# Kernel optimization log

Hardware: AMD Instinct MI355X
Metric: run time of the kernel (lower is better)

Reference implementation:

```python
import jax, jax.numpy as jnp
import numpy as np


def _quantize(m):
    # per-row symmetric int8 quantization: absmax over last dim, round to nearest-even
    max_val = jnp.max(jnp.abs(m), axis=-1)          # [...]
    q = jnp.round(m * (127.0 / max_val)[..., None])  # values in [-127, 127], kept in fp32
    return q, max_val


def setup_inputs() -> dict:
    key = jax.random.key(0)
    k1, k2, k3 = jax.random.split(key, 3)
    B, S, D_IN, D_OUT = 4, 8192, 1024, 1024
    x = jax.random.normal(k1, (B, S, D_IN), dtype=jnp.float32)
    weight = jax.random.normal(k2, (D_OUT, D_IN), dtype=jnp.float32) * 0.02
    bias = jax.random.normal(k3, (D_OUT,), dtype=jnp.float32)
    return {"x": x, "weight": weight, "bias": bias}


def reference(x, weight, bias):
    # weight quantization happens once in __init__; replicated here for self-containment
    w_q, w_max = _quantize(weight)    # [N,K], [N]
    x_q, x_max = _quantize(x)         # [B,S,K], [B,S]
    # int8 GEMM emulated in fp32, exactly as the original module does
    res_q = jnp.einsum('bsk,nk->bsn', x_q, w_q)            # [B,S,N] fp32
    mx = x_max[..., None] * w_max                          # outer-product dequant scale [B,S,N]
    res = (res_q / (127.0 * 127.0)).astype(jnp.float16) * mx  # fp16 * fp32 -> fp32
    return res + bias
```

## Files before the change

### kernel.cpp

```cpp
#include <hip/hip_runtime.h>
#include <hip/hip_fp16.h>


typedef int i32x4 __attribute__((ext_vector_type(4)));

#define BM 128
#define BN 128
#define BKB 128

__global__ __launch_bounds__(256) void quant_rows_kernel(
    const float* __restrict__ in, signed char* __restrict__ q,
    float* __restrict__ rowmax, int K, int R) {
  const int row = blockIdx.x;
  const int t = threadIdx.x;
  const size_t base = (size_t)row * K;
  float4 v = reinterpret_cast<const float4*>(in + base)[t];
  float a = fmaxf(fmaxf(fabsf(v.x), fabsf(v.y)), fmaxf(fabsf(v.z), fabsf(v.w)));
#pragma unroll
  for (int off = 32; off > 0; off >>= 1) a = fmaxf(a, __shfl_xor(a, off, 64));
  __shared__ float smax[4];
  if ((t & 63) == 0) smax[t >> 6] = a;
  __syncthreads();
  float m = fmaxf(fmaxf(smax[0], smax[1]), fmaxf(smax[2], smax[3]));
  float s = 127.0f / m;
  char4 qq;
  qq.x = (signed char)(int)rintf(v.x * s);
  qq.y = (signed char)(int)rintf(v.y * s);
  qq.z = (signed char)(int)rintf(v.z * s);
  qq.w = (signed char)(int)rintf(v.w * s);
  const int kb = t >> 5;
  signed char* dst =
      q + (size_t)kb * R * BKB + (size_t)row * BKB + (t & 31) * 4;
  *reinterpret_cast<char4*>(dst) = qq;
  if (t == 0) rowmax[row] = m;
}

__device__ __forceinline__ void gload_lds16(const void* g, void* l) {
  __builtin_amdgcn_global_load_lds(
      (const __attribute__((address_space(1))) unsigned char*)g,
      (__attribute__((address_space(3))) unsigned char*)l, 16, 0, 0);
}

__global__ __launch_bounds__(256) void w8x8_gemm_kernel(
    const signed char* __restrict__ Aq, const signed char* __restrict__ Bq,
    const float* __restrict__ Amax, const float* __restrict__ Bmax,
    const float* __restrict__ bias, float* __restrict__ out,
    int M, int N, int K, int cpx) {
  __shared__ __align__(16) signed char ldsA[2][BM * BKB];
  __shared__ __align__(16) signed char ldsB[2][BN * BKB];
  const int t = threadIdx.x;
  const int lane = t & 63;
  const int wave = t >> 6;
  const int wrow = wave >> 1, wcol = wave & 1;

  const int nbn = N / BN;
  const int bid = blockIdx.x;
  const int tile = (bid & 7) * cpx + (bid >> 3);
  const int bm = tile / nbn, bn = tile % nbn;

  const size_t kbStrideA = (size_t)M * BKB;
  const size_t kbStrideB = (size_t)N * BKB;
  const signed char* Abase = Aq + (size_t)bm * BM * BKB;
  const signed char* Bbase = Bq + (size_t)bn * BN * BKB;

  const int soff = (t * 16) ^ (((t >> 3) & 7) << 4);

  const int fr = lane & 15, fq = lane >> 4;
  int aoff[4][2], boff[4][2];
#pragma unroll
  for (int m = 0; m < 4; ++m) {
    int ra = wrow * 64 + m * 16 + fr;
    int rb = wcol * 64 + m * 16 + fr;
#pragma unroll
    for (int ks = 0; ks < 2; ++ks) {
      aoff[m][ks] = ra * BKB + (((ks << 2) | fq) ^ (ra & 7)) * 16;
      boff[m][ks] = rb * BKB + (((ks << 2) | fq) ^ (rb & 7)) * 16;
    }
  }

  i32x4 acc[4][4];
#pragma unroll
  for (int m = 0; m < 4; ++m)
#pragma unroll
    for (int n = 0; n < 4; ++n) acc[m][n] = (i32x4){0, 0, 0, 0};

#define STAGE(bf, kt)                                                        \
  do {                                                                       \
    const signed char* ga = Abase + (size_t)(kt)*kbStrideA;                  \
    const signed char* gb = Bbase + (size_t)(kt)*kbStrideB;                  \
    gload_lds16(ga + soff, &ldsA[bf][t * 16]);                               \
    gload_lds16(ga + 4096 + soff, &ldsA[bf][4096 + t * 16]);                 \
    gload_lds16(ga + 8192 + soff, &ldsA[bf][8192 + t * 16]);                 \
    gload_lds16(ga + 12288 + soff, &ldsA[bf][12288 + t * 16]);               \
    gload_lds16(gb + soff, &ldsB[bf][t * 16]);                               \
    gload_lds16(gb + 4096 + soff, &ldsB[bf][4096 + t * 16]);                 \
    gload_lds16(gb + 8192 + soff, &ldsB[bf][8192 + t * 16]);                 \
    gload_lds16(gb + 12288 + soff, &ldsB[bf][12288 + t * 16]);               \
  } while (0)

  const int NT = K / BKB;
  STAGE(0, 0);
  asm volatile("s_waitcnt vmcnt(0)" ::: "memory");
  __builtin_amdgcn_s_barrier();

  for (int kt = 0; kt < NT; ++kt) {
    const signed char* lA = ldsA[kt & 1];
    const signed char* lB = ldsB[kt & 1];
    const bool pf = (kt + 1 < NT);
    if (pf) STAGE((kt + 1) & 1, kt + 1);

#pragma unroll
    for (int ks = 0; ks < 2; ++ks) {
      i32x4 a[4], b[4];
#pragma unroll
      for (int m = 0; m < 4; ++m) {
        a[m] = *reinterpret_cast<const i32x4*>(lA + aoff[m][ks]);
        b[m] = *reinterpret_cast<const i32x4*>(lB + boff[m][ks]);
      }
      __builtin_amdgcn_s_setprio(1);
#pragma unroll
      for (int m = 0; m < 4; ++m)
#pragma unroll
        for (int n = 0; n < 4; ++n)
          acc[m][n] = __builtin_amdgcn_mfma_i32_16x16x64_i8(a[m], b[n],
                                                            acc[m][n], 0, 0, 0);
      __builtin_amdgcn_s_setprio(0);
    }

    if (pf) {
      asm volatile("s_waitcnt vmcnt(0)" ::: "memory");
      __builtin_amdgcn_s_barrier();
    }
  }
#undef STAGE

  const int row0 = bm * BM + wrow * 64;
  const int col0 = bn * BN + wcol * 64;
  const float C = 1.0f / 16129.0f;
  float wmx[4], bs[4];
#pragma unroll
  for (int n = 0; n < 4; ++n) {
    int col = col0 + n * 16 + fr;
    wmx[n] = Bmax[col];
    bs[n] = bias[col];
  }
#pragma unroll
  for (int m = 0; m < 4; ++m) {
#pragma unroll
    for (int r = 0; r < 4; ++r) {
      int row = row0 + m * 16 + fq * 4 + r;
      float xm = Amax[row];
      float* orow = out + (size_t)row * N;
#pragma unroll
      for (int n = 0; n < 4; ++n) {
        float v = (float)acc[m][n][r] * C;
        float h = __half2float(__float2half_rn(v));
        orow[col0 + n * 16 + fr] = h * (xm * wmx[n]) + bs[n];
      }
    }
  }
}

extern "C" void kernel_launch(void* const* d_in, const int* in_sizes, int n_in,
                              void* d_out, int out_size, void* d_ws, size_t ws_size,
                              hipStream_t stream) {
  const float* x = (const float*)d_in[0];
  const float* w = (const float*)d_in[1];
  const float* bias = (const float*)d_in[2];
  float* out = (float*)d_out;

  const int N = in_sizes[2];
  const int K = in_sizes[1] / N;
  const int M = in_sizes[0] / K;

  signed char* xq = (signed char*)d_ws;
  signed char* wq = xq + (size_t)M * K;
  float* xmax = (float*)(wq + (size_t)N * K);
  float* wmax = xmax + M;

  quant_rows_kernel<<<M, 256, 0, stream>>>(x, xq, xmax, K, M);
  quant_rows_kernel<<<N, 256, 0, stream>>>(w, wq, wmax, K, N);

  const int nwg = (M / BM) * (N / BN);
  const int cpx = nwg / 8;
  w8x8_gemm_kernel<<<nwg, 256, 0, stream>>>(xq, wq, xmax, wmax, bias, out,
                                            M, N, K, cpx);
}
```

Before: 95.12 us.

## Use 256x256 tiles, 8 waves, triple-buffered K=64 pipeline with interleaved prefetch

Tiles grow to 256x256 with 512 threads. Each wave computes a 64x128 sub-tile, and the K step shrinks to 64 bytes. Shared memory now holds three buffers, with loads issued two K-steps ahead and split into A and B halves that are interleaved between MFMA groups under barriers. The quantized layout is rebuilt for 64-byte K blocks. This aims at better operand reuse and keeping the matrix units fed, at the cost of more barriers, higher register pressure and lower occupancy.

```diff
diff --git a/kernel.cpp b/kernel.cpp
--- a/kernel.cpp
+++ b/kernel.cpp
@@ -4,9 +4,9 @@
 
 typedef int i32x4 __attribute__((ext_vector_type(4)));
 
-#define BM 128
-#define BN 128
-#define BKB 128
+#define BM 256
+#define BN 256
+#define KB 64
 
 __global__ __launch_bounds__(256) void quant_rows_kernel(
     const float* __restrict__ in, signed char* __restrict__ q,
@@ -28,9 +28,8 @@
   qq.y = (signed char)(int)rintf(v.y * s);
   qq.z = (signed char)(int)rintf(v.z * s);
   qq.w = (signed char)(int)rintf(v.w * s);
-  const int kb = t >> 5;
-  signed char* dst =
-      q + (size_t)kb * R * BKB + (size_t)row * BKB + (t & 31) * 4;
+  const int kb = t >> 4;
+  signed char* dst = q + (size_t)kb * R * KB + (size_t)row * KB + (t & 15) * 4;
   *reinterpret_cast<char4*>(dst) = qq;
   if (t == 0) rowmax[row] = m;
 }
@@ -41,105 +40,147 @@
       (__attribute__((address_space(3))) unsigned char*)l, 16, 0, 0);
 }
 
-__global__ __launch_bounds__(256) void w8x8_gemm_kernel(
+__global__ __launch_bounds__(512) void w8x8_gemm_kernel(
     const signed char* __restrict__ Aq, const signed char* __restrict__ Bq,
     const float* __restrict__ Amax, const float* __restrict__ Bmax,
     const float* __restrict__ bias, float* __restrict__ out,
     int M, int N, int K, int cpx) {
-  __shared__ __align__(16) signed char ldsA[2][BM * BKB];
-  __shared__ __align__(16) signed char ldsB[2][BN * BKB];
+  __shared__ __align__(16) signed char ldsA[3][BM * KB];
+  __shared__ __align__(16) signed char ldsB[3][BN * KB];
   const int t = threadIdx.x;
   const int lane = t & 63;
   const int wave = t >> 6;
-  const int wrow = wave >> 1, wcol = wave & 1;
+  const int wm = wave >> 1;
+  const int wn = wave & 1;
 
   const int nbn = N / BN;
   const int bid = blockIdx.x;
   const int tile = (bid & 7) * cpx + (bid >> 3);
   const int bm = tile / nbn, bn = tile % nbn;
 
-  const size_t kbStrideA = (size_t)M * BKB;
-  const size_t kbStrideB = (size_t)N * BKB;
-  const signed char* Abase = Aq + (size_t)bm * BM * BKB;
-  const signed char* Bbase = Bq + (size_t)bn * BN * BKB;
-
-  const int soff = (t * 16) ^ (((t >> 3) & 7) << 4);
+  const size_t kbA = (size_t)M * KB;
+  const size_t kbB = (size_t)N * KB;
+  const signed char* Abase = Aq + (size_t)bm * BM * KB;
+  const signed char* Bbase = Bq + (size_t)bn * BN * KB;
+
+  const int ssoff = (t * 16) ^ (((t >> 3) & 3) << 4);
+  const int sdst = t * 16;
 
   const int fr = lane & 15, fq = lane >> 4;
-  int aoff[4][2], boff[4][2];
-#pragma unroll
-  for (int m = 0; m < 4; ++m) {
-    int ra = wrow * 64 + m * 16 + fr;
-    int rb = wcol * 64 + m * 16 + fr;
-#pragma unroll
-    for (int ks = 0; ks < 2; ++ks) {
-      aoff[m][ks] = ra * BKB + (((ks << 2) | fq) ^ (ra & 7)) * 16;
-      boff[m][ks] = rb * BKB + (((ks << 2) | fq) ^ (rb & 7)) * 16;
-    }
+  const int xr = (fr >> 1) & 3;
+  int aoff[4], boff[8];
+#pragma unroll
+  for (int m = 0; m < 4; ++m)
+    aoff[m] = (wm * 64 + m * 16 + fr) * KB + ((fq ^ xr) << 4);
+#pragma unroll
+  for (int n = 0; n < 8; ++n)
+    boff[n] = (wn * 128 + n * 16 + fr) * KB + ((fq ^ xr) << 4);
+
+  i32x4 acc[4][8];
+#pragma unroll
+  for (int m = 0; m < 4; ++m)
+#pragma unroll
+    for (int n = 0; n < 8; ++n) acc[m][n] = (i32x4){0, 0, 0, 0};
+
+#define STAGE_A(bf, kt)                                                    \
+  do {                                                                    \
+    const signed char* ga = Abase + (size_t)(kt) * kbA;                   \
+    gload_lds16(ga + ssoff, &ldsA[bf][sdst]);                             \
+    gload_lds16(ga + 8192 + ssoff, &ldsA[bf][8192 + sdst]);               \
+  } while (0)
+#define STAGE_B(bf, kt)                                                    \
+  do {                                                                    \
+    const signed char* gb = Bbase + (size_t)(kt) * kbB;                   \
+    gload_lds16(gb + ssoff, &ldsB[bf][sdst]);                             \
+    gload_lds16(gb + 8192 + ssoff, &ldsB[bf][8192 + sdst]);               \
+  } while (0)
+
+  const int NT = K / KB;
+  STAGE_A(0, 0);
+  STAGE_B(0, 0);
+  STAGE_A(1, 1);
+  STAGE_B(1, 1);
+  asm volatile("s_waitcnt vmcnt(4)" ::: "memory");
+  __builtin_amdgcn_s_barrier();
+
+  int cb = 0;
+  for (int kt = 0; kt < NT; ++kt) {
+    const signed char* lA = ldsA[cb];
+    const signed char* lB = ldsB[cb];
+    int sb = cb + 2;
+    if (sb >= 3) sb -= 3;
+    const bool p2 = (kt + 2 < NT), p1 = (kt + 1 < NT);
+
+    i32x4 a[4], b0, b1;
+#pragma unroll
+    for (int m = 0; m < 4; ++m)
+      a[m] = *reinterpret_cast<const i32x4*>(lA + aoff[m]);
+    b0 = *reinterpret_cast<const i32x4*>(lB + boff[0]);
+    b1 = *reinterpret_cast<const i32x4*>(lB + boff[1]);
+    if (p2) STAGE_A(sb, kt + 2);
+    __builtin_amdgcn_s_barrier();
+    __builtin_amdgcn_s_setprio(1);
+#pragma unroll
+    for (int m = 0; m < 4; ++m) {
+      acc[m][0] = __builtin_amdgcn_mfma_i32_16x16x64_i8(a[m], b0, acc[m][0], 0, 0, 0);
+      acc[m][1] = __builtin_amdgcn_mfma_i32_16x16x64_i8(a[m], b1, acc[m][1], 0, 0, 0);
+    }
+    __builtin_amdgcn_s_setprio(0);
+    __builtin_amdgcn_s_barrier();
+
+    b0 = *reinterpret_cast<const i32x4*>(lB + boff[2]);
+    b1 = *reinterpret_cast<const i32x4*>(lB + boff[3]);
+    if (p2) STAGE_B(sb, kt + 2);
+    __builtin_amdgcn_s_barrier();
+    __builtin_amdgcn_s_setprio(1);
+#pragma unroll
+    for (int m = 0; m < 4; ++m) {
+      acc[m][2] = __builtin_amdgcn_mfma_i32_16x16x64_i8(a[m], b0, acc[m][2], 0, 0, 0);
+      acc[m][3] = __builtin_amdgcn_mfma_i32_16x16x64_i8(a[m], b1, acc[m][3], 0, 0, 0);
+    }
+    __builtin_amdgcn_s_setprio(0);
+    __builtin_amdgcn_s_barrier();
+
+    b0 = *reinterpret_cast<const i32x4*>(lB + boff[4]);
+    b1 = *reinterpret_cast<const i32x4*>(lB + boff[5]);
+    __builtin_amdgcn_s_barrier();
+    __builtin_amdgcn_s_setprio(1);
+#pragma unroll
+    for (int m = 0; m < 4; ++m) {
+      acc[m][4] = __builtin_amdgcn_mfma_i32_16x16x64_i8(a[m], b0, acc[m][4], 0, 0, 0);
+      acc[m][5] = __builtin_amdgcn_mfma_i32_16x16x64_i8(a[m], b1, acc[m][5], 0, 0, 0);
+    }
+    __builtin_amdgcn_s_setprio(0);
+    __builtin_amdgcn_s_barrier();
+
+    b0 = *reinterpret_cast<const i32x4*>(lB + boff[6]);
+    b1 = *reinterpret_cast<const i32x4*>(lB + boff[7]);
+    __builtin_amdgcn_s_barrier();
+    __builtin_amdgcn_s_setprio(1);
+#pragma unroll
+    for (int m = 0; m < 4; ++m) {
+      acc[m][6] = __builtin_amdgcn_mfma_i32_16x16x64_i8(a[m], b0, acc[m][6], 0, 0, 0);
+      acc[m][7] = __builtin_amdgcn_mfma_i32_16x16x64_i8(a[m], b1, acc[m][7], 0, 0, 0);
+    }
+    __builtin_amdgcn_s_setprio(0);
+    if (p1) {
+      if (p2)
+        asm volatile("s_waitcnt vmcnt(4)" ::: "memory");
+      else
+        asm volatile("s_waitcnt vmcnt(0)" ::: "memory");
+    }
+    __builtin_amdgcn_s_barrier();
+    cb = (cb + 1 == 3) ? 0 : cb + 1;
   }
-
-  i32x4 acc[4][4];
-#pragma unroll
-  for (int m = 0; m < 4; ++m)
-#pragma unroll
-    for (int n = 0; n < 4; ++n) acc[m][n] = (i32x4){0, 0, 0, 0};
-
-#define STAGE(bf, kt)                                                        \
-  do {                                                                       \
-    const signed char* ga = Abase + (size_t)(kt)*kbStrideA;                  \
-    const signed char* gb = Bbase + (size_t)(kt)*kbStrideB;                  \
-    gload_lds16(ga + soff, &ldsA[bf][t * 16]);                               \
-    gload_lds16(ga + 4096 + soff, &ldsA[bf][4096 + t * 16]);                 \
-    gload_lds16(ga + 8192 + soff, &ldsA[bf][8192 + t * 16]);                 \
-    gload_lds16(ga + 12288 + soff, &ldsA[bf][12288 + t * 16]);               \
-    gload_lds16(gb + soff, &ldsB[bf][t * 16]);                               \
-    gload_lds16(gb + 4096 + soff, &ldsB[bf][4096 + t * 16]);                 \
-    gload_lds16(gb + 8192 + soff, &ldsB[bf][8192 + t * 16]);                 \
-    gload_lds16(gb + 12288 + soff, &ldsB[bf][12288 + t * 16]);               \
-  } while (0)
-
-  const int NT = K / BKB;
-  STAGE(0, 0);
-  asm volatile("s_waitcnt vmcnt(0)" ::: "memory");
-  __builtin_amdgcn_s_barrier();
-
-  for (int kt = 0; kt < NT; ++kt) {
-    const signed char* lA = ldsA[kt & 1];
-    const signed char* lB = ldsB[kt & 1];
-    const bool pf = (kt + 1 < NT);
-    if (pf) STAGE((kt + 1) & 1, kt + 1);
-
-#pragma unroll
-    for (int ks = 0; ks < 2; ++ks) {
-      i32x4 a[4], b[4];
-#pragma unroll
-      for (int m = 0; m < 4; ++m) {
-        a[m] = *reinterpret_cast<const i32x4*>(lA + aoff[m][ks]);
-        b[m] = *reinterpret_cast<const i32x4*>(lB + boff[m][ks]);
-      }
-      __builtin_amdgcn_s_setprio(1);
-#pragma unroll
-      for (int m = 0; m < 4; ++m)
-#pragma unroll
-        for (int n = 0; n < 4; ++n)
-          acc[m][n] = __builtin_amdgcn_mfma_i32_16x16x64_i8(a[m], b[n],
-                                                            acc[m][n], 0, 0, 0);
-      __builtin_amdgcn_s_setprio(0);
-    }
-
-    if (pf) {
-      asm volatile("s_waitcnt vmcnt(0)" ::: "memory");
-      __builtin_amdgcn_s_barrier();
-    }
-  }
-#undef STAGE
-
-  const int row0 = bm * BM + wrow * 64;
-  const int col0 = bn * BN + wcol * 64;
+#undef STAGE_A
+#undef STAGE_B
+
+  const int row0 = bm * BM + wm * 64;
+  const int col0 = bn * BN + wn * 128;
   const float C = 1.0f / 16129.0f;
-  float wmx[4], bs[4];
-#pragma unroll
-  for (int n = 0; n < 4; ++n) {
+  float wmx[8], bs[8];
+#pragma unroll
+  for (int n = 0; n < 8; ++n) {
     int col = col0 + n * 16 + fr;
     wmx[n] = Bmax[col];
     bs[n] = bias[col];
@@ -152,7 +193,7 @@
       float xm = Amax[row];
       float* orow = out + (size_t)row * N;
 #pragma unroll
-      for (int n = 0; n < 4; ++n) {
+      for (int n = 0; n < 8; ++n) {
         float v = (float)acc[m][n][r] * C;
         float h = __half2float(__float2half_rn(v));
         orow[col0 + n * 16 + fr] = h * (xm * wmx[n]) + bs[n];
@@ -183,6 +224,6 @@
 
   const int nwg = (M / BM) * (N / BN);
   const int cpx = nwg / 8;
-  w8x8_gemm_kernel<<<nwg, 256, 0, stream>>>(xq, wq, xmax, wmax, bias, out,
+  w8x8_gemm_kernel<<<nwg, 512, 0, stream>>>(xq, wq, xmax, wmax, bias, out,
                                             M, N, K, cpx);
 }
```

Result: slower. 98.77 us (+3.8%).
